# Kernel tuning notes

Measured on AMD Instinct MI355X. Metric: run time of the kernel, lower is better.

Reference implementation:

```python
import jax, jax.numpy as jnp
import numpy as np

CODE_NUM = 12288
GRAPH = 128      # graph_size: embedding width / GRU input
HIDDEN = 128     # GRU hidden = t_output_size = time_size (required by scatter/broadcast)
ATT = 64         # t_attention_size


def setup_inputs() -> dict:
    key = jax.random.key(0)
    ks = jax.random.split(key, 20)
    s = 0.05
    # disjoint 3-way membership masks (m1/m2/m3), some codes in no set
    cat = jax.random.randint(ks[0], (CODE_NUM,), 0, 4)
    divided = jax.nn.one_hot(cat, 4, dtype=jnp.int32)[:, :3]
    return {
        "interval": jnp.asarray(3.5, jnp.float32),
        "co_embeddings": jax.random.normal(ks[1], (CODE_NUM, GRAPH), jnp.float32),
        "no_embeddings": jax.random.normal(ks[2], (CODE_NUM, GRAPH), jnp.float32),
        "unrelated_embeddings": jax.random.normal(ks[3], (CODE_NUM, GRAPH), jnp.float32),
        "hidden_state": jax.random.normal(ks[4], (CODE_NUM, HIDDEN), jnp.float32),
        "divided": divided,
        # GRUCell params (torch layout: [3H, in], gates r|z|n)
        "W_ih": jax.random.normal(ks[5], (3 * HIDDEN, GRAPH), jnp.float32) * s,
        "W_hh": jax.random.normal(ks[6], (3 * HIDDEN, HIDDEN), jnp.float32) * s,
        "b_ih": jax.random.normal(ks[7], (3 * HIDDEN,), jnp.float32) * s,
        "b_hh": jax.random.normal(ks[8], (3 * HIDDEN,), jnp.float32) * s,
        # SingleHeadAttentionLayer params
        "Wq": jax.random.normal(ks[9], (ATT, GRAPH), jnp.float32) * s,
        "bq": jax.random.normal(ks[10], (ATT,), jnp.float32) * s,
        "Wk": jax.random.normal(ks[11], (ATT, GRAPH), jnp.float32) * s,
        "bk": jax.random.normal(ks[12], (ATT,), jnp.float32) * s,
        "Wv": jax.random.normal(ks[13], (HIDDEN, GRAPH), jnp.float32) * s,
        "bv": jax.random.normal(ks[14], (HIDDEN,), jnp.float32) * s,
        # time_layer: Linear(1, time_size)
        "Wt": jax.random.normal(ks[15], (HIDDEN, 1), jnp.float32) * s,
        "bt": jax.random.normal(ks[16], (HIDDEN,), jnp.float32) * s,
        "t": 1,
        "is_last": 0,
    }


def _gru_cell(x, h, W_ih, W_hh, b_ih, b_hh):
    gi = x @ W_ih.T + b_ih          # [N, 3H]
    gh = h @ W_hh.T + b_hh          # [N, 3H]
    i_r, i_z, i_n = jnp.split(gi, 3, axis=-1)
    h_r, h_z, h_n = jnp.split(gh, 3, axis=-1)
    r = jax.nn.sigmoid(i_r + h_r)
    z = jax.nn.sigmoid(i_z + h_z)
    n = jnp.tanh(i_n + r * h_n)
    return (1.0 - z) * n + z * h


def reference(interval, co_embeddings, no_embeddings, unrelated_embeddings,
              hidden_state, divided, W_ih, W_hh, b_ih, b_hh,
              Wq, bq, Wk, bk, Wv, bv, Wt, bt, t, is_last):
    dt = co_embeddings.dtype
    # time feature: tanh(Linear(1/log(interval + e)))
    x_t = 1.0 / jnp.log(interval + jnp.e)                       # scalar
    time_features = jnp.tanh(x_t * Wt[:, 0] + bt)               # [H]

    if is_last:
        out = _gru_cell(co_embeddings, hidden_state, W_ih, W_hh, b_ih, b_hh)
        return (out + time_features, None)

    m1 = divided[:, 0] > 0
    m2 = divided[:, 1] > 0
    m3 = divided[:, 2] > 0
    m23 = m2 | m3
    NEG = jnp.finfo(dt).min

    # --- m1 branch: GRUCell is row-wise, so compute on all rows and mask ---
    h_gru = _gru_cell(co_embeddings, hidden_state, W_ih, W_hh, b_ih, b_hh)  # [N, H]
    output_m1 = jnp.max(jnp.where(m1[:, None], h_gru, NEG), axis=0)        # [H]

    # --- m2/m3 branch: attention over the m23 subset (mask-based, order-free)
    # query rows: m2 -> no_embeddings, m3 -> unrelated_embeddings
    q_full = jnp.where(m2[:, None], no_embeddings, unrelated_embeddings)   # [N, G]
    Q = q_full @ Wq.T + bq                                                 # [N, A]
    K = co_embeddings @ Wk.T + bk                                          # [N, A]
    V = co_embeddings @ Wv.T + bv                                          # [N, H]
    scores = (Q @ K.T) / jnp.sqrt(jnp.asarray(ATT, dt))                    # [N, N]
    scores = jnp.where(m23[None, :], scores, NEG)                          # keys restricted to m23
    attn = jax.nn.softmax(scores, axis=-1)
    h_att = jnp.tanh(attn @ V)                                             # [N, H]
    output_m23 = jnp.max(jnp.where(m23[:, None], h_att, NEG), axis=0)      # [H]

    # scatter: m2/m3 rows written after m1 rows (m23 takes precedence)
    h_new = jnp.where(m23[:, None], h_att,
                      jnp.where(m1[:, None], h_gru, jnp.zeros((), dt)))

    output = jnp.maximum(output_m1, output_m23)
    return (output + time_features, h_new)
```

## Files before the change

kernel.cpp:

```cpp
#include <hip/hip_runtime.h>
#include <hip/hip_bf16.h>
#include <math.h>

#define N_CODES 12288
#define G 128
#define H 128
#define ATT 64
#define NEGF (-3.4028234663852886e38f)
#define NSEG 8
#define QT 32
#define QMAX 7168
#define NQTA (QMAX / QT)

typedef __attribute__((ext_vector_type(8))) short bf16x8;
typedef __attribute__((ext_vector_type(4))) float f32x4;
typedef __hip_bfloat16 bf16;
#define MFMA16(a, b, c) __builtin_amdgcn_mfma_f32_16x16x32_bf16(a, b, c, 0, 0, 0)

struct __align__(16) Ws {
  int n1;
  int n23;
  int cnt;
  int pad_;
  int idx1[N_CODES];
  int rows23[N_CODES];
  int flags23[N_CODES];
  unsigned maxu[128];
  float tf[128];
  float lseg[NSEG * QMAX];
  float bqkv[256];
  float b2[512];
  bf16 Wqkv[16 * 4 * 64 * 8];
  bf16 W2[32 * 8 * 64 * 8];
  bf16 Qb[(size_t)N_CODES * ATT];
  bf16 Kf[(size_t)N_CODES * ATT];
  bf16 Vf[(size_t)N_CODES * H];
  bf16 Oseg[(size_t)NSEG * QMAX * H];
};

__device__ inline uint2 pack4(float4 v) {
  union { bf16 b[4]; uint2 u; } cv;
  cv.b[0] = __float2bfloat16(v.x);
  cv.b[1] = __float2bfloat16(v.y);
  cv.b[2] = __float2bfloat16(v.z);
  cv.b[3] = __float2bfloat16(v.w);
  return cv.u;
}

__device__ inline float bf2f(short s) {
  union { unsigned u; float f; } c;
  c.u = ((unsigned)(unsigned short)s) << 16;
  return c.f;
}

__device__ inline unsigned fkey(float f) {
  unsigned b = __float_as_uint(f);
  return (b & 0x80000000u) ? ~b : (b | 0x80000000u);
}
__device__ inline float funkey(unsigned u) {
  unsigned b = (u & 0x80000000u) ? (u & 0x7fffffffu) : ~u;
  return __uint_as_float(b);
}

__global__ void k_setup(const int* __restrict__ divided,
                        const float* __restrict__ Wq, const float* __restrict__ bq,
                        const float* __restrict__ Wk, const float* __restrict__ bk,
                        const float* __restrict__ Wv, const float* __restrict__ bv,
                        const float* __restrict__ W_ih, const float* __restrict__ W_hh,
                        const float* __restrict__ b_ih, const float* __restrict__ b_hh,
                        const float* __restrict__ interval, const float* __restrict__ Wt,
                        const float* __restrict__ bt, Ws* ws, float* __restrict__ h_new) {
  int bid = blockIdx.x;
  int t = threadIdx.x;
  if (bid < 48) {
    int r = bid * 256 + t;
    int m1 = divided[r * 3 + 0] > 0;
    int m2 = divided[r * 3 + 1] > 0;
    int m3 = divided[r * 3 + 2] > 0;
    if (m1) {
      int p = atomicAdd(&ws->n1, 1);
      ws->idx1[p] = r;
    }
    if (m2 | m3) {
      int p = atomicAdd(&ws->n23, 1);
      ws->rows23[p] = r;
      ws->flags23[p] = m2;
    }
    if (!(m1 | m2 | m3)) {
      float4 z = {0.f, 0.f, 0.f, 0.f};
      float4* hr = (float4*)&h_new[(size_t)r * H];
#pragma unroll
      for (int i = 0; i < 32; ++i) hr[i] = z;
    }
    return;
  }
  if (bid < 80) {
    int idx = (bid - 48) * 256 + t;
    int c = idx >> 5, k = (idx & 31) * 4;
    float4 v;
    if (c < 64) {
      v = *(const float4*)&Wq[c * G + k];
      v.x *= 0.125f; v.y *= 0.125f; v.z *= 0.125f; v.w *= 0.125f;
    } else if (c < 128) {
      v = *(const float4*)&Wk[(c - 64) * G + k];
    } else {
      v = *(const float4*)&Wv[(c - 128) * G + k];
    }
    int NB = c >> 4, lo = c & 15, ks = k >> 5, hi = (k >> 3) & 3, j = k & 7;
    *(uint2*)&ws->Wqkv[((NB * 4 + ks) * 64 + hi * 16 + lo) * 8 + j] = pack4(v);
    return;
  }
  if (bid < 208) {
    int idx = (bid - 80) * 256 + t;
    int c = idx >> 6, k = (idx & 63) * 4;
    int g = c >> 7, d = c & 127;
    float4 v = {0.f, 0.f, 0.f, 0.f};
    if (g == 0) v = (k < 128) ? *(const float4*)&W_ih[d * G + k]
                              : *(const float4*)&W_hh[d * H + (k - 128)];
    else if (g == 1) v = (k < 128) ? *(const float4*)&W_ih[(128 + d) * G + k]
                                   : *(const float4*)&W_hh[(128 + d) * H + (k - 128)];
    else if (g == 2) { if (k < 128) v = *(const float4*)&W_ih[(256 + d) * G + k]; }
    else { if (k >= 128) v = *(const float4*)&W_hh[(256 + d) * H + (k - 128)]; }
    int NB = c >> 4, lo = c & 15, ks = k >> 5, hi = (k >> 3) & 3, j = k & 7;
    *(uint2*)&ws->W2[((NB * 8 + ks) * 64 + hi * 16 + lo) * 8 + j] = pack4(v);
    return;
  }
  if (t < 128) {
    float xt = 1.0f / logf(interval[0] + 2.718281828459045f);
    ws->tf[t] = tanhf(xt * Wt[t] + bt[t]);
    ws->maxu[t] = 0u;
  }
  for (int i = t; i < 768; i += 256) {
    if (i < 256) {
      float v;
      if (i < 64) v = bq[i] * 0.125f;
      else if (i < 128) v = bk[i - 64];
      else v = bv[i - 128];
      ws->bqkv[i] = v;
    } else {
      int c = i - 256;
      int g = c >> 7, d = c & 127;
      float v;
      if (g == 0) v = b_ih[d] + b_hh[d];
      else if (g == 1) v = b_ih[128 + d] + b_hh[128 + d];
      else if (g == 2) v = b_ih[256 + d];
      else v = b_hh[256 + d];
      ws->b2[c] = v;
    }
  }
}

__launch_bounds__(256)
__global__ void k_mm(const float* __restrict__ co, const float* __restrict__ no_e,
                     const float* __restrict__ un_e, const float* __restrict__ hs,
                     Ws* ws, float* __restrict__ h_new) {
  __shared__ __align__(16) bf16 sm[8704];
  int bid = blockIdx.x;
  int t = threadIdx.x;
  int w = t >> 6, lane = t & 63, lo = lane & 15, hi = lane >> 4;

  if (bid < 768) {
    int n23 = ws->n23;
    int q0 = (bid >> 1) * 16;
    int z = bid & 1;
    if (q0 >= n23) return;
    bf16(*Aq)[136] = (bf16(*)[136])sm;
    bf16(*Ac)[136] = (bf16(*)[136])(sm + 2176);
    for (int it = 0; it < 2; ++it) {
      int idx = it * 256 + t;
      int rr = idx >> 5, c4 = idx & 31;
      uint2 pq = {0, 0}, pc = {0, 0};
      int p = q0 + rr;
      if (p < n23) {
        int row = ws->rows23[p];
        pc = pack4(*(const float4*)&co[(size_t)row * G + c4 * 4]);
        if (z == 0) {
          const float* srcq = ws->flags23[p] ? no_e : un_e;
          pq = pack4(*(const float4*)&srcq[(size_t)row * G + c4 * 4]);
        }
      }
      if (z == 0) *(uint2*)&Aq[rr][c4 * 4] = pq;
      *(uint2*)&Ac[rr][c4 * 4] = pc;
    }
    __syncthreads();
    const bf16(*At)[136] = (z == 0 && w < 2) ? Aq : Ac;
    f32x4 acc[2];
#pragma unroll
    for (int nb = 0; nb < 2; ++nb) acc[nb] = (f32x4){0.f, 0.f, 0.f, 0.f};
#pragma unroll
    for (int ks = 0; ks < 4; ++ks) {
      bf16x8 af = *(const bf16x8*)&At[lo][ks * 32 + hi * 8];
#pragma unroll
      for (int nb = 0; nb < 2; ++nb) {
        int NBg = z * 8 + w * 2 + nb;
        bf16x8 bfr = *(const bf16x8*)&ws->Wqkv[((NBg * 4 + ks) * 64 + lane) * 8];
        acc[nb] = MFMA16(af, bfr, acc[nb]);
      }
    }
#pragma unroll
    for (int nb = 0; nb < 2; ++nb) {
      int c = z * 128 + w * 32 + nb * 16 + lo;
      float bias = ws->bqkv[c];
#pragma unroll
      for (int r = 0; r < 4; ++r) {
        int p = q0 + hi * 4 + r;
        if (p >= n23) continue;
        bf16 bv16 = __float2bfloat16(acc[nb][r] + bias);
        if (c < 64) {
          ws->Qb[(size_t)p * ATT + c] = bv16;
        } else if (c < 128) {
          int d = c - 64;
          ws->Kf[(((p >> 4) * 2 + (d >> 5)) * 64 + ((d >> 3) & 3) * 16 + (p & 15)) * 8 + (d & 7)] = bv16;
        } else {
          int d = c - 128;
          ws->Vf[((((p >> 6) * 8 + (d >> 4)) * 2 + ((p >> 5) & 1)) * 64 + ((p >> 3) & 3) * 16 + (d & 15)) * 8 + (p & 7)] = bv16;
        }
      }
    }
  } else {
    int n1 = ws->n1;
    int q0 = ((bid - 768) >> 1) * 16;
    int z = bid & 1;
    if (q0 >= n1) return;
    bf16(*A2)[264] = (bf16(*)[264])sm;
    for (int it = 0; it < 4; ++it) {
      int idx = it * 256 + t;
      int rr = idx >> 6, c4 = idx & 63;
      uint2 pk = {0, 0};
      int p = q0 + rr;
      if (p < n1) {
        int row = ws->idx1[p];
        float4 v = (c4 < 32) ? *(const float4*)&co[(size_t)row * G + c4 * 4]
                             : *(const float4*)&hs[(size_t)row * H + (c4 - 32) * 4];
        pk = pack4(v);
      }
      *(uint2*)&A2[rr][c4 * 4] = pk;
    }
    __syncthreads();
    f32x4 acc[4];
#pragma unroll
    for (int g = 0; g < 4; ++g) acc[g] = (f32x4){0.f, 0.f, 0.f, 0.f};
#pragma unroll
    for (int ks = 0; ks < 8; ++ks) {
      bf16x8 af = *(const bf16x8*)&A2[lo][ks * 32 + hi * 8];
#pragma unroll
      for (int g = 0; g < 4; ++g) {
        int NB = g * 8 + z * 4 + w;
        bf16x8 bfr = *(const bf16x8*)&ws->W2[((NB * 8 + ks) * 64 + lane) * 8];
        acc[g] = MFMA16(af, bfr, acc[g]);
      }
    }
    int d = z * 64 + w * 16 + lo;
    float br = ws->b2[d], bz = ws->b2[128 + d], bin_ = ws->b2[256 + d], bhn = ws->b2[384 + d];
    float mx = NEGF;
#pragma unroll
    for (int r = 0; r < 4; ++r) {
      int p = q0 + hi * 4 + r;
      if (p >= n1) continue;
      int row = ws->idx1[p];
      float rs = acc[0][r] + br;
      float zs = acc[1][r] + bz;
      float in_ = acc[2][r] + bin_;
      float hn = acc[3][r] + bhn;
      float rg = 1.f / (1.f + __expf(-rs));
      float zg = 1.f / (1.f + __expf(-zs));
      float ng = tanhf(in_ + rg * hn);
      float h0 = hs[(size_t)row * H + d];
      float hv = (1.f - zg) * ng + zg * h0;
      h_new[(size_t)row * H + d] = hv;
      mx = fmaxf(mx, hv);
    }
    mx = fmaxf(mx, __shfl_xor(mx, 16));
    mx = fmaxf(mx, __shfl_xor(mx, 32));
    if (hi == 0) atomicMax(&ws->maxu[d], fkey(mx));
  }
}

__launch_bounds__(256)
__global__ void k_attn(const Ws* __restrict__ ws, Ws* __restrict__ wso) {
  int n23 = ws->n23;
  int bid = blockIdx.x;
  int q0 = (bid % NQTA) * QT;
  int seg = bid / NQTA;
  if (q0 >= n23) return;
  int segk = (((n23 + NSEG - 1) / NSEG) + 63) & ~63;
  int s0 = seg * segk;
  int t = threadIdx.x;
  if (s0 >= n23) {
    for (int idx = t; idx < QT * 32; idx += 256) {
      int q = q0 + (idx >> 5);
      if (q < n23) {
        uint2 z2 = {0, 0};
        *(uint2*)&wso->Oseg[((size_t)seg * QMAX + q) * H + (idx & 31) * 4] = z2;
      }
    }
    if (t < QT && q0 + t < n23) wso->lseg[seg * QMAX + q0 + t] = 0.f;
    return;
  }
  int send = min(s0 + segk, n23);

  int w = t >> 6, lane = t & 63, lo = lane & 15, hi = lane >> 4;

  __shared__ bf16 Pl[32][72];
  __shared__ float Lw[4][32];

  bf16x8 qf[2][2];
#pragma unroll
  for (int qsub = 0; qsub < 2; ++qsub)
#pragma unroll
    for (int s = 0; s < 2; ++s)
      qf[qsub][s] =
          *(const bf16x8*)&ws->Qb[(size_t)(q0 + qsub * 16 + lo) * ATT + s * 32 + hi * 8];

  f32x4 acc[2][2];
#pragma unroll
  for (int ddl = 0; ddl < 2; ++ddl)
#pragma unroll
    for (int qsub = 0; qsub < 2; ++qsub) acc[ddl][qsub] = (f32x4){0.f, 0.f, 0.f, 0.f};
  float lacc[2] = {0.f, 0.f};

  for (int c0 = s0; c0 < send; c0 += 64) {
    int kb = (c0 >> 4) + w;
    bf16x8 kf0 = *(const bf16x8*)&ws->Kf[((size_t)(kb * 2 + 0) * 64 + lane) * 8];
    bf16x8 kf1 = *(const bf16x8*)&ws->Kf[((size_t)(kb * 2 + 1) * 64 + lane) * 8];
#pragma unroll
    for (int qsub = 0; qsub < 2; ++qsub) {
      f32x4 s_ = {0.f, 0.f, 0.f, 0.f};
      s_ = MFMA16(kf0, qf[qsub][0], s_);
      s_ = MFMA16(kf1, qf[qsub][1], s_);
      union { bf16 b[4]; uint2 u; } tu;
      float sl = 0.f;
#pragma unroll
      for (int r = 0; r < 4; ++r) {
        int key = c0 + w * 16 + hi * 4 + r;
        float p = (key < send) ? __expf(s_[r]) : 0.f;
        sl += p;
        tu.b[r] = __float2bfloat16(p);
      }
      *(uint2*)&Pl[qsub * 16 + lo][w * 16 + hi * 4] = tu.u;
      sl += __shfl_xor(sl, 16);
      sl += __shfl_xor(sl, 32);
      lacc[qsub] += sl;
    }
    __syncthreads();

    int kc = c0 >> 6;
    bf16x8 vf[2][2];
#pragma unroll
    for (int s = 0; s < 2; ++s)
#pragma unroll
      for (int ddl = 0; ddl < 2; ++ddl)
        vf[s][ddl] =
            *(const bf16x8*)&ws->Vf[((size_t)(kc * 16 + (w * 2 + ddl) * 2 + s) * 64 + lane) * 8];
#pragma unroll
    for (int s = 0; s < 2; ++s) {
      bf16x8 pf[2];
#pragma unroll
      for (int qsub = 0; qsub < 2; ++qsub)
        pf[qsub] = *(const bf16x8*)&Pl[qsub * 16 + lo][s * 32 + hi * 8];
#pragma unroll
      for (int ddl = 0; ddl < 2; ++ddl)
#pragma unroll
        for (int qsub = 0; qsub < 2; ++qsub)
          acc[ddl][qsub] = MFMA16(vf[s][ddl], pf[qsub], acc[ddl][qsub]);
    }
    __syncthreads();
  }

  if (hi == 0) {
#pragma unroll
    for (int qsub = 0; qsub < 2; ++qsub) Lw[w][qsub * 16 + lo] = lacc[qsub];
  }
  __syncthreads();
  if (t < QT) {
    int q = q0 + t;
    if (q < n23) wso->lseg[seg * QMAX + q] = Lw[0][t] + Lw[1][t] + Lw[2][t] + Lw[3][t];
  }
#pragma unroll
  for (int qsub = 0; qsub < 2; ++qsub) {
    int q = q0 + qsub * 16 + lo;
    if (q < n23) {
#pragma unroll
      for (int ddl = 0; ddl < 2; ++ddl) {
        union { bf16 b[4]; uint2 u; } tmp;
#pragma unroll
        for (int r = 0; r < 4; ++r) tmp.b[r] = __float2bfloat16(acc[ddl][qsub][r]);
        *(uint2*)&wso->Oseg[((size_t)seg * QMAX + q) * H + w * 32 + ddl * 16 + hi * 4] = tmp.u;
      }
    }
  }
}

__global__ void k_merge(const Ws* __restrict__ ws, float* __restrict__ h_new, Ws* wso,
                        float* __restrict__ out) {
  int n23 = ws->n23;
  int qb = blockIdx.x * 16;
  if (qb >= n23) return;
  int t = threadIdx.x;
  int ql = t >> 4, d8 = (t & 15) * 8;
  int q = qb + ql;

  __shared__ float red[16][128];
  float h8[8];
  bool act = q < n23;
  if (act) {
    float o[8];
#pragma unroll
    for (int j = 0; j < 8; ++j) o[j] = 0.f;
    float L = 0.f;
#pragma unroll
    for (int s = 0; s < NSEG; ++s) {
      bf16x8 ov = *(const bf16x8*)&ws->Oseg[((size_t)s * QMAX + q) * H + d8];
#pragma unroll
      for (int j = 0; j < 8; ++j) o[j] += bf2f(ov[j]);
      L += ws->lseg[s * QMAX + q];
    }
    float linv = 1.0f / L;
    float4 h0, h1;
#pragma unroll
    for (int j = 0; j < 8; ++j) h8[j] = tanhf(o[j] * linv);
    h0.x = h8[0]; h0.y = h8[1]; h0.z = h8[2]; h0.w = h8[3];
    h1.x = h8[4]; h1.y = h8[5]; h1.z = h8[6]; h1.w = h8[7];
    float* hr = &h_new[(size_t)ws->rows23[q] * H + d8];
    *(float4*)hr = h0;
    *(float4*)(hr + 4) = h1;
  } else {
#pragma unroll
    for (int j = 0; j < 8; ++j) h8[j] = NEGF;
  }
#pragma unroll
  for (int j = 0; j < 8; ++j) red[ql][d8 + j] = h8[j];
  __syncthreads();
  if (t < 128) {
    float m = NEGF;
#pragma unroll
    for (int ql2 = 0; ql2 < 16; ++ql2) m = fmaxf(m, red[ql2][t]);
    atomicMax(&wso->maxu[t], fkey(m));
  }
  __shared__ int lastv;
  __syncthreads();
  if (t == 0) {
    __threadfence();
    int nact = (n23 + 15) >> 4;
    lastv = (atomicAdd(&wso->cnt, 1) == nact - 1) ? 1 : 0;
  }
  __syncthreads();
  if (lastv && t < 128) {
    unsigned u = atomicOr(&wso->maxu[t], 0u);
    out[t] = funkey(u) + ws->tf[t];
  }
}

extern "C" void kernel_launch(void* const* d_in, const int* in_sizes, int n_in,
                              void* d_out, int out_size, void* d_ws, size_t ws_size,
                              hipStream_t stream) {
  const float* interval = (const float*)d_in[0];
  const float* co = (const float*)d_in[1];
  const float* no_e = (const float*)d_in[2];
  const float* un_e = (const float*)d_in[3];
  const float* hs = (const float*)d_in[4];
  const int* divided = (const int*)d_in[5];
  const float* W_ih = (const float*)d_in[6];
  const float* W_hh = (const float*)d_in[7];
  const float* b_ih = (const float*)d_in[8];
  const float* b_hh = (const float*)d_in[9];
  const float* Wq = (const float*)d_in[10];
  const float* bq = (const float*)d_in[11];
  const float* Wk = (const float*)d_in[12];
  const float* bk = (const float*)d_in[13];
  const float* Wv = (const float*)d_in[14];
  const float* bv = (const float*)d_in[15];
  const float* Wt = (const float*)d_in[16];
  const float* bt = (const float*)d_in[17];

  float* out = (float*)d_out;
  float* h_new = out + 128;
  Ws* ws = (Ws*)d_ws;

  hipMemsetAsync(ws, 0, 16, stream);

  k_setup<<<209, 256, 0, stream>>>(divided, Wq, bq, Wk, bk, Wv, bv, W_ih, W_hh, b_ih, b_hh,
                                   interval, Wt, bt, ws, h_new);
  k_mm<<<1536, 256, 0, stream>>>(co, no_e, un_e, hs, ws, h_new);
  k_attn<<<NQTA * NSEG, 256, 0, stream>>>(ws, ws);
  k_merge<<<(QMAX + 15) / 16, 256, 0, stream>>>(ws, h_new, ws, out);
}
```

Measured before the change: 180.2 us.

## Fuse split-K merge into attention kernel via per-query-tile arrival counters

Removes the separate merge kernel. Each attention block bumps a per-query-tile counter after writing its partial output and row sum, and the last of the NSEG segment blocks for that tile reduces the partials, applies tanh, scatters into h_new and updates the global max. This saves one kernel launch and lets merging overlap with remaining attention work. In exchange it adds fences and atomics, and each block now reserves a 16KB shared reduction buffer, which may lower occupancy.

```diff
diff --git a/kernel.cpp b/kernel.cpp
--- a/kernel.cpp
+++ b/kernel.cpp
@@ -22,6 +22,7 @@
   int n23;
   int cnt;
   int pad_;
+  int qcnt[252];
   int idx1[N_CODES];
   int rows23[N_CODES];
   int flags23[N_CODES];
@@ -277,15 +278,25 @@
 }
 
 __launch_bounds__(256)
-__global__ void k_attn(const Ws* __restrict__ ws, Ws* __restrict__ wso) {
+__global__ void k_attn(const Ws* __restrict__ ws, Ws* __restrict__ wso,
+                       float* __restrict__ h_new, float* __restrict__ out) {
   int n23 = ws->n23;
   int bid = blockIdx.x;
-  int q0 = (bid % NQTA) * QT;
+  int qi = bid % NQTA;
+  int q0 = qi * QT;
   int seg = bid / NQTA;
   if (q0 >= n23) return;
   int segk = (((n23 + NSEG - 1) / NSEG) + 63) & ~63;
   int s0 = seg * segk;
   int t = threadIdx.x;
+  int w = t >> 6, lane = t & 63, lo = lane & 15, hi = lane >> 4;
+
+  __shared__ bf16 Pl[32][72];
+  __shared__ float Lw[4][32];
+  __shared__ float red[32][128];
+  __shared__ float Ls[32];
+  __shared__ int lastv, lastq;
+
   if (s0 >= n23) {
     for (int idx = t; idx < QT * 32; idx += 256) {
       int q = q0 + (idx >> 5);
@@ -295,157 +306,159 @@
       }
     }
     if (t < QT && q0 + t < n23) wso->lseg[seg * QMAX + q0 + t] = 0.f;
-    return;
-  }
-  int send = min(s0 + segk, n23);
-
-  int w = t >> 6, lane = t & 63, lo = lane & 15, hi = lane >> 4;
-
-  __shared__ bf16 Pl[32][72];
-  __shared__ float Lw[4][32];
-
-  bf16x8 qf[2][2];
-#pragma unroll
-  for (int qsub = 0; qsub < 2; ++qsub)
-#pragma unroll
-    for (int s = 0; s < 2; ++s)
-      qf[qsub][s] =
-          *(const bf16x8*)&ws->Qb[(size_t)(q0 + qsub * 16 + lo) * ATT + s * 32 + hi * 8];
-
-  f32x4 acc[2][2];
-#pragma unroll
-  for (int ddl = 0; ddl < 2; ++ddl)
-#pragma unroll
-    for (int qsub = 0; qsub < 2; ++qsub) acc[ddl][qsub] = (f32x4){0.f, 0.f, 0.f, 0.f};
-  float lacc[2] = {0.f, 0.f};
-
-  for (int c0 = s0; c0 < send; c0 += 64) {
-    int kb = (c0 >> 4) + w;
-    bf16x8 kf0 = *(const bf16x8*)&ws->Kf[((size_t)(kb * 2 + 0) * 64 + lane) * 8];
-    bf16x8 kf1 = *(const bf16x8*)&ws->Kf[((size_t)(kb * 2 + 1) * 64 + lane) * 8];
+  } else {
+    int send = min(s0 + segk, n23);
+
+    bf16x8 qf[2][2];
+#pragma unroll
+    for (int qsub = 0; qsub < 2; ++qsub)
+#pragma unroll
+      for (int s = 0; s < 2; ++s)
+        qf[qsub][s] =
+            *(const bf16x8*)&ws->Qb[(size_t)(q0 + qsub * 16 + lo) * ATT + s * 32 + hi * 8];
+
+    f32x4 acc[2][2];
+#pragma unroll
+    for (int ddl = 0; ddl < 2; ++ddl)
+#pragma unroll
+      for (int qsub = 0; qsub < 2; ++qsub) acc[ddl][qsub] = (f32x4){0.f, 0.f, 0.f, 0.f};
+    float lacc[2] = {0.f, 0.f};
+
+    for (int c0 = s0; c0 < send; c0 += 64) {
+      int kb = (c0 >> 4) + w;
+      bf16x8 kf0 = *(const bf16x8*)&ws->Kf[((size_t)(kb * 2 + 0) * 64 + lane) * 8];
+      bf16x8 kf1 = *(const bf16x8*)&ws->Kf[((size_t)(kb * 2 + 1) * 64 + lane) * 8];
+#pragma unroll
+      for (int qsub = 0; qsub < 2; ++qsub) {
+        f32x4 s_ = {0.f, 0.f, 0.f, 0.f};
+        s_ = MFMA16(kf0, qf[qsub][0], s_);
+        s_ = MFMA16(kf1, qf[qsub][1], s_);
+        union { bf16 b[4]; uint2 u; } tu;
+        float sl = 0.f;
+#pragma unroll
+        for (int r = 0; r < 4; ++r) {
+          int key = c0 + w * 16 + hi * 4 + r;
+          float p = (key < send) ? __expf(s_[r]) : 0.f;
+          sl += p;
+          tu.b[r] = __float2bfloat16(p);
+        }
+        *(uint2*)&Pl[qsub * 16 + lo][w * 16 + hi * 4] = tu.u;
+        sl += __shfl_xor(sl, 16);
+        sl += __shfl_xor(sl, 32);
+        lacc[qsub] += sl;
+      }
+      __syncthreads();
+
+      int kc = c0 >> 6;
+      bf16x8 vf[2][2];
+#pragma unroll
+      for (int s = 0; s < 2; ++s)
+#pragma unroll
+        for (int ddl = 0; ddl < 2; ++ddl)
+          vf[s][ddl] =
+              *(const bf16x8*)&ws->Vf[((size_t)(kc * 16 + (w * 2 + ddl) * 2 + s) * 64 + lane) * 8];
+#pragma unroll
+      for (int s = 0; s < 2; ++s) {
+        bf16x8 pf[2];
+#pragma unroll
+        for (int qsub = 0; qsub < 2; ++qsub)
+          pf[qsub] = *(const bf16x8*)&Pl[qsub * 16 + lo][s * 32 + hi * 8];
+#pragma unroll
+        for (int ddl = 0; ddl < 2; ++ddl)
+#pragma unroll
+          for (int qsub = 0; qsub < 2; ++qsub)
+            acc[ddl][qsub] = MFMA16(vf[s][ddl], pf[qsub], acc[ddl][qsub]);
+      }
+      __syncthreads();
+    }
+
+    if (hi == 0) {
+#pragma unroll
+      for (int qsub = 0; qsub < 2; ++qsub) Lw[w][qsub * 16 + lo] = lacc[qsub];
+    }
+    __syncthreads();
+    if (t < QT) {
+      int q = q0 + t;
+      if (q < n23) wso->lseg[seg * QMAX + q] = Lw[0][t] + Lw[1][t] + Lw[2][t] + Lw[3][t];
+    }
 #pragma unroll
     for (int qsub = 0; qsub < 2; ++qsub) {
-      f32x4 s_ = {0.f, 0.f, 0.f, 0.f};
-      s_ = MFMA16(kf0, qf[qsub][0], s_);
-      s_ = MFMA16(kf1, qf[qsub][1], s_);
-      union { bf16 b[4]; uint2 u; } tu;
-      float sl = 0.f;
-#pragma unroll
-      for (int r = 0; r < 4; ++r) {
-        int key = c0 + w * 16 + hi * 4 + r;
-        float p = (key < send) ? __expf(s_[r]) : 0.f;
-        sl += p;
-        tu.b[r] = __float2bfloat16(p);
-      }
-      *(uint2*)&Pl[qsub * 16 + lo][w * 16 + hi * 4] = tu.u;
-      sl += __shfl_xor(sl, 16);
-      sl += __shfl_xor(sl, 32);
-      lacc[qsub] += sl;
-    }
-    __syncthreads();
-
-    int kc = c0 >> 6;
-    bf16x8 vf[2][2];
-#pragma unroll
-    for (int s = 0; s < 2; ++s)
-#pragma unroll
-      for (int ddl = 0; ddl < 2; ++ddl)
-        vf[s][ddl] =
-            *(const bf16x8*)&ws->Vf[((size_t)(kc * 16 + (w * 2 + ddl) * 2 + s) * 64 + lane) * 8];
-#pragma unroll
-    for (int s = 0; s < 2; ++s) {
-      bf16x8 pf[2];
-#pragma unroll
-      for (int qsub = 0; qsub < 2; ++qsub)
-        pf[qsub] = *(const bf16x8*)&Pl[qsub * 16 + lo][s * 32 + hi * 8];
-#pragma unroll
-      for (int ddl = 0; ddl < 2; ++ddl)
-#pragma unroll
-        for (int qsub = 0; qsub < 2; ++qsub)
-          acc[ddl][qsub] = MFMA16(vf[s][ddl], pf[qsub], acc[ddl][qsub]);
-    }
-    __syncthreads();
-  }
-
-  if (hi == 0) {
-#pragma unroll
-    for (int qsub = 0; qsub < 2; ++qsub) Lw[w][qsub * 16 + lo] = lacc[qsub];
-  }
-  __syncthreads();
+      int q = q0 + qsub * 16 + lo;
+      if (q < n23) {
+#pragma unroll
+        for (int ddl = 0; ddl < 2; ++ddl) {
+          union { bf16 b[4]; uint2 u; } tmp;
+#pragma unroll
+          for (int r = 0; r < 4; ++r) tmp.b[r] = __float2bfloat16(acc[ddl][qsub][r]);
+          *(uint2*)&wso->Oseg[((size_t)seg * QMAX + q) * H + w * 32 + ddl * 16 + hi * 4] = tmp.u;
+        }
+      }
+    }
+  }
+
+  __threadfence();
+  __syncthreads();
+  if (t == 0) lastv = (atomicAdd(&wso->qcnt[qi], 1) == NSEG - 1) ? 1 : 0;
+  __syncthreads();
+  if (!lastv) return;
+
   if (t < QT) {
     int q = q0 + t;
-    if (q < n23) wso->lseg[seg * QMAX + q] = Lw[0][t] + Lw[1][t] + Lw[2][t] + Lw[3][t];
-  }
-#pragma unroll
-  for (int qsub = 0; qsub < 2; ++qsub) {
-    int q = q0 + qsub * 16 + lo;
+    float L = 0.f;
     if (q < n23) {
 #pragma unroll
-      for (int ddl = 0; ddl < 2; ++ddl) {
-        union { bf16 b[4]; uint2 u; } tmp;
-#pragma unroll
-        for (int r = 0; r < 4; ++r) tmp.b[r] = __float2bfloat16(acc[ddl][qsub][r]);
-        *(uint2*)&wso->Oseg[((size_t)seg * QMAX + q) * H + w * 32 + ddl * 16 + hi * 4] = tmp.u;
-      }
-    }
-  }
-}
-
-__global__ void k_merge(const Ws* __restrict__ ws, float* __restrict__ h_new, Ws* wso,
-                        float* __restrict__ out) {
-  int n23 = ws->n23;
-  int qb = blockIdx.x * 16;
-  if (qb >= n23) return;
-  int t = threadIdx.x;
-  int ql = t >> 4, d8 = (t & 15) * 8;
-  int q = qb + ql;
-
-  __shared__ float red[16][128];
-  float h8[8];
-  bool act = q < n23;
-  if (act) {
-    float o[8];
-#pragma unroll
-    for (int j = 0; j < 8; ++j) o[j] = 0.f;
-    float L = 0.f;
-#pragma unroll
-    for (int s = 0; s < NSEG; ++s) {
-      bf16x8 ov = *(const bf16x8*)&ws->Oseg[((size_t)s * QMAX + q) * H + d8];
-#pragma unroll
-      for (int j = 0; j < 8; ++j) o[j] += bf2f(ov[j]);
-      L += ws->lseg[s * QMAX + q];
-    }
-    float linv = 1.0f / L;
-    float4 h0, h1;
-#pragma unroll
-    for (int j = 0; j < 8; ++j) h8[j] = tanhf(o[j] * linv);
-    h0.x = h8[0]; h0.y = h8[1]; h0.z = h8[2]; h0.w = h8[3];
-    h1.x = h8[4]; h1.y = h8[5]; h1.z = h8[6]; h1.w = h8[7];
-    float* hr = &h_new[(size_t)ws->rows23[q] * H + d8];
-    *(float4*)hr = h0;
-    *(float4*)(hr + 4) = h1;
-  } else {
-#pragma unroll
-    for (int j = 0; j < 8; ++j) h8[j] = NEGF;
-  }
-#pragma unroll
-  for (int j = 0; j < 8; ++j) red[ql][d8 + j] = h8[j];
+      for (int s = 0; s < NSEG; ++s) L += wso->lseg[s * QMAX + q];
+      Ls[t] = 1.0f / L;
+    } else {
+      Ls[t] = 0.f;
+    }
+  }
+  __syncthreads();
+  for (int u = t; u < QT * 16; u += 256) {
+    int ql = u >> 4, d8 = (u & 15) * 8;
+    int q = q0 + ql;
+    float h8[8];
+    if (q < n23) {
+      float o[8];
+#pragma unroll
+      for (int j = 0; j < 8; ++j) o[j] = 0.f;
+#pragma unroll
+      for (int s = 0; s < NSEG; ++s) {
+        bf16x8 ov = *(const bf16x8*)&wso->Oseg[((size_t)s * QMAX + q) * H + d8];
+#pragma unroll
+        for (int j = 0; j < 8; ++j) o[j] += bf2f(ov[j]);
+      }
+      float linv = Ls[ql];
+#pragma unroll
+      for (int j = 0; j < 8; ++j) h8[j] = tanhf(o[j] * linv);
+      float4 h0, h1;
+      h0.x = h8[0]; h0.y = h8[1]; h0.z = h8[2]; h0.w = h8[3];
+      h1.x = h8[4]; h1.y = h8[5]; h1.z = h8[6]; h1.w = h8[7];
+      float* hr = &h_new[(size_t)ws->rows23[q] * H + d8];
+      *(float4*)hr = h0;
+      *(float4*)(hr + 4) = h1;
+    } else {
+#pragma unroll
+      for (int j = 0; j < 8; ++j) h8[j] = NEGF;
+    }
+#pragma unroll
+    for (int j = 0; j < 8; ++j) red[ql][d8 + j] = h8[j];
+  }
   __syncthreads();
   if (t < 128) {
     float m = NEGF;
 #pragma unroll
-    for (int ql2 = 0; ql2 < 16; ++ql2) m = fmaxf(m, red[ql2][t]);
+    for (int ql2 = 0; ql2 < QT; ++ql2) m = fmaxf(m, red[ql2][t]);
     atomicMax(&wso->maxu[t], fkey(m));
   }
-  __shared__ int lastv;
+  __threadfence();
   __syncthreads();
   if (t == 0) {
-    __threadfence();
-    int nact = (n23 + 15) >> 4;
-    lastv = (atomicAdd(&wso->cnt, 1) == nact - 1) ? 1 : 0;
-  }
-  __syncthreads();
-  if (lastv && t < 128) {
+    int nqt = (n23 + QT - 1) / QT;
+    lastq = (atomicAdd(&wso->cnt, 1) == nqt - 1) ? 1 : 0;
+  }
+  __syncthreads();
+  if (lastq && t < 128) {
     unsigned u = atomicOr(&wso->maxu[t], 0u);
     out[t] = funkey(u) + ws->tf[t];
   }
@@ -477,11 +490,10 @@
   float* h_new = out + 128;
   Ws* ws = (Ws*)d_ws;
 
-  hipMemsetAsync(ws, 0, 16, stream);
+  hipMemsetAsync(ws, 0, 1024, stream);
 
   k_setup<<<209, 256, 0, stream>>>(divided, Wq, bq, Wk, bk, Wv, bv, W_ih, W_hh, b_ih, b_hh,
                                    interval, Wt, bt, ws, h_new);
   k_mm<<<1536, 256, 0, stream>>>(co, no_e, un_e, hs, ws, h_new);
-  k_attn<<<NQTA * NSEG, 256, 0, stream>>>(ws, ws);
-  k_merge<<<(QMAX + 15) / 16, 256, 0, stream>>>(ws, h_new, ws, out);
-}
+  k_attn<<<NQTA * NSEG, 256, 0, stream>>>(ws, ws, h_new, out);
+}
```

New measurement: 356.7 us. +97.9%, slower.
